# Kernel optimization log

Hardware: AMD Instinct MI355X
Metric: run time of the kernel (lower is better)

The kernel has to match this reference:

```python
import jax, jax.numpy as jnp
import numpy as np

N = 50000   # num nodes
E = 800000  # num edges
D = 128     # embedding dim
EPS = 1e-5


def setup_inputs() -> dict:
    key = jax.random.key(0)
    ks = jax.random.split(key, 16)
    x = jnp.arange(N, dtype=jnp.int32)
    edge_index = jax.random.randint(ks[0], (2, E), 0, N, dtype=jnp.int32)
    weight = jax.random.uniform(ks[1], (E,), dtype=jnp.float32)
    emb = jax.random.normal(ks[2], (N, D), dtype=jnp.float32)
    # layer dims: 128->128, 128->64, 64->32
    dims = [(128, 128), (128, 64), (64, 32)]
    inp = {"x": x, "edge_index": edge_index, "weight": weight, "emb": emb}
    for i, (fi, fo) in enumerate(dims, start=1):
        s = 1.0 / np.sqrt(fi)
        inp[f"W{i}"] = jax.random.uniform(ks[3 * i], (fi, fo), dtype=jnp.float32, minval=-s, maxval=s)
        inp[f"b{i}"] = jnp.zeros((fo,), dtype=jnp.float32)
        inp[f"g{i}"] = jnp.ones((fo,), dtype=jnp.float32)
        inp[f"be{i}"] = jnp.zeros((fo,), dtype=jnp.float32)
    return inp


def _gcn_conv(h, src, dst, w, W, b):
    # PyG GCNConv: linear, add self-loops (weight 1), symmetric normalization, scatter-add
    h = h @ W  # [N, Fout]
    loop = jnp.arange(N, dtype=src.dtype)
    src_l = jnp.concatenate([src, loop])
    dst_l = jnp.concatenate([dst, loop])
    w_l = jnp.concatenate([w, jnp.ones((N,), w.dtype)])
    deg = jax.ops.segment_sum(w_l, dst_l, num_segments=N)
    dinv = jnp.where(deg > 0, jax.lax.rsqrt(jnp.maximum(deg, 1e-30)), 0.0)
    norm = dinv[src_l] * w_l * dinv[dst_l]  # [E+N]
    msg = h[src_l] * norm[:, None]          # gather + scale, [E+N, Fout]
    out = jax.ops.segment_sum(msg, dst_l, num_segments=N)
    return out + b


def _batch_norm(h, g, be):
    mu = h.mean(axis=0)
    var = h.var(axis=0)  # biased, as torch BN uses for normalization
    return (h - mu) * jax.lax.rsqrt(var + EPS) * g + be


def reference(x, edge_index, weight, emb,
              W1, b1, g1, be1,
              W2, b2, g2, be2,
              W3, b3, g3, be3):
    src, dst = edge_index[0], edge_index[1]
    h = emb[x]  # embedding lookup
    h = _batch_norm(_gcn_conv(h, src, dst, weight, W1, b1), g1, be1)
    h = jax.nn.relu(h)
    h = _batch_norm(_gcn_conv(h, src, dst, weight, W2, b2), g2, be2)
    h = jax.nn.relu(h)
    h = _batch_norm(_gcn_conv(h, src, dst, weight, W3, b3), g3, be3)
    return h
```

## Files before the change

### kernel.cpp

```cpp
#include <hip/hip_runtime.h>
#include <hip/hip_bf16.h>

#define BN_EPS 1e-5f
#define FIXSCALE 16777216.0f
#define FIXINV   5.9604644775390625e-08
#define LOWMASK  0xFFFFFFFFFFULL

typedef __attribute__((ext_vector_type(8))) short bf16x8;
typedef __attribute__((ext_vector_type(4))) float f32x4;

__device__ __forceinline__ unsigned short bfu(float v) {
  return __bfloat16_as_ushort(__float2bfloat16(v));
}
__device__ __forceinline__ unsigned int pk_bf2(float a, float b) {
  return (unsigned int)bfu(a) | ((unsigned int)bfu(b) << 16);
}
__device__ __forceinline__ float bf_lo(unsigned int u) { return __uint_as_float(u << 16); }
__device__ __forceinline__ float bf_hi(unsigned int u) { return __uint_as_float(u & 0xFFFF0000u); }

__device__ __forceinline__ void fma8(float* a, uint4 u, float c) {
  a[0] += bf_lo(u.x) * c; a[1] += bf_hi(u.x) * c;
  a[2] += bf_lo(u.y) * c; a[3] += bf_hi(u.y) * c;
  a[4] += bf_lo(u.z) * c; a[5] += bf_hi(u.z) * c;
  a[6] += bf_lo(u.w) * c; a[7] += bf_hi(u.w) * c;
}

__device__ __forceinline__ float4 load4(const float* p) { return *(const float4*)p; }
__device__ __forceinline__ float4 load4(const unsigned short* p) {
  uint2 u = *(const uint2*)p;
  return make_float4(bf_lo(u.x), bf_hi(u.x), bf_lo(u.y), bf_hi(u.y));
}


__global__ void prep_k(const float* __restrict__ W1, const float* __restrict__ W2,
                       const float* __restrict__ W3, unsigned short* __restrict__ wt1,
                       unsigned short* __restrict__ wt2, unsigned short* __restrict__ wt3,
                       unsigned long long* __restrict__ packed, int n) {
  int idx = blockIdx.x * 256 + threadIdx.x;
  if (idx < n) packed[idx] = 0ULL;
  if (idx < 128 * 128) {
    int c = idx >> 7, k = idx & 127;
    wt1[idx] = bfu(W1[k * 128 + c]);
  } else if (idx < 128 * 128 + 128 * 64) {
    int i2 = idx - 128 * 128;
    int c = i2 >> 7, k = i2 & 127;
    wt2[i2] = bfu(W2[k * 64 + c]);
  } else if (idx < 128 * 128 + 128 * 64 + 64 * 32) {
    int i2 = idx - 128 * 128 - 128 * 64;
    int c = i2 >> 6, k = i2 & 63;
    wt3[i2] = bfu(W3[k * 32 + c]);
  }
}


__global__ void hist64_k(const int* __restrict__ dst, const float* __restrict__ w,
                         unsigned long long* __restrict__ packed, int* __restrict__ rank, int e) {
  int i = (blockIdx.x * blockDim.x + threadIdx.x) * 2;
  if (i + 1 < e) {
    int2 d2 = *(const int2*)(dst + i);
    float2 w2 = *(const float2*)(w + i);
    unsigned long long a0 = (1ULL << 40) | (unsigned long long)__float2uint_rn(w2.x * FIXSCALE);
    unsigned long long a1 = (1ULL << 40) | (unsigned long long)__float2uint_rn(w2.y * FIXSCALE);
    unsigned long long o0 = atomicAdd(&packed[d2.x], a0);
    unsigned long long o1 = atomicAdd(&packed[d2.y], a1);
    *(int2*)(rank + i) = make_int2((int)(o0 >> 40), (int)(o1 >> 40));
  } else if (i < e) {
    unsigned long long fw = (unsigned long long)__float2uint_rn(w[i] * FIXSCALE);
    unsigned long long old = atomicAdd(&packed[dst[i]], (1ULL << 40) | fw);
    rank[i] = (int)(old >> 40);
  }
}

__global__ void scan_partial_k(const unsigned long long* __restrict__ packed,
                               int* __restrict__ bsum, float* __restrict__ dinv, int n) {
  __shared__ int s[256];
  int idx = blockIdx.x * 256 + threadIdx.x;
  unsigned long long p = (idx < n) ? packed[idx] : 0ULL;
  if (idx < n)
    dinv[idx] = rsqrtf(1.0f + (float)((double)(p & LOWMASK) * FIXINV));
  s[threadIdx.x] = (int)(p >> 40);
  __syncthreads();
  for (int off = 128; off > 0; off >>= 1) {
    if (threadIdx.x < off) s[threadIdx.x] += s[threadIdx.x + off];
    __syncthreads();
  }
  if (threadIdx.x == 0) bsum[blockIdx.x] = s[0];
}

__global__ void scan_final_k(const unsigned long long* __restrict__ packed,
                             const int* __restrict__ bsum, int* __restrict__ rowptr,
                             int n, int nb) {
  __shared__ int sb[256];
  __shared__ int s[256];
  const int b = blockIdx.x, t = threadIdx.x;

  int bv = (t < nb) ? bsum[t] : 0;
  sb[t] = bv;
  __syncthreads();
  for (int off = 1; off < 256; off <<= 1) {
    int u = (t >= off) ? sb[t - off] : 0;
    __syncthreads();
    sb[t] += u;
    __syncthreads();
  }
  const int blockbase = (b == 0) ? 0 : sb[b - 1];
  if (b == 0 && t == 0) rowptr[n] = sb[nb - 1];

  int idx = b * 256 + t;
  int v = (idx < n) ? (int)(packed[idx] >> 40) : 0;
  s[t] = v;
  __syncthreads();
  for (int off = 1; off < 256; off <<= 1) {
    int u = (t >= off) ? s[t - off] : 0;
    __syncthreads();
    s[t] += u;
    __syncthreads();
  }
  if (idx < n) rowptr[idx] = blockbase + s[t] - v;
}

__global__ void scatter_nb_k(const int* __restrict__ src, const int* __restrict__ dst,
                             const float* __restrict__ w, const int* __restrict__ rank,
                             const float* __restrict__ dinv, const int* __restrict__ rowptr,
                             int2* __restrict__ csr, int e) {
  int i = (blockIdx.x * blockDim.x + threadIdx.x) * 2;
  if (i + 1 < e) {
    int2 s2 = *(const int2*)(src + i);
    int2 d2 = *(const int2*)(dst + i);
    float2 w2 = *(const float2*)(w + i);
    int2 r2 = *(const int2*)(rank + i);
    int p0 = rowptr[d2.x] + r2.x;
    int p1 = rowptr[d2.y] + r2.y;
    csr[p0] = make_int2(s2.x, __float_as_int(dinv[s2.x] * w2.x * dinv[d2.x]));
    csr[p1] = make_int2(s2.y, __float_as_int(dinv[s2.y] * w2.y * dinv[d2.y]));
  } else if (i < e) {
    int d = dst[i], s = src[i];
    int pos = rowptr[d] + rank[i];
    csr[pos] = make_int2(s, __float_as_int(dinv[s] * w[i] * dinv[d]));
  }
}


template <typename TIN, int FIN, int FOUT, bool BNIN, bool GATHER>
__global__ __launch_bounds__(256) void gemm_mfma_k(
    const TIN* __restrict__ H, const int* __restrict__ xidx,
    const float* __restrict__ scale, const float* __restrict__ shift,
    const unsigned short* __restrict__ WtG, unsigned short* __restrict__ out, int n) {
  constexpr int C4 = FIN / 4;
  constexpr int ldH = FIN + 8;
  constexpr int ldW = FIN + 8;
  constexpr int ldC = FOUT + 4;
  constexpr int NCT = FOUT / 16;
  constexpr int NK = FIN / 32;
  constexpr int HT_SH = 64 * ldH;
  constexpr int WT_SH = FOUT * ldW;
  constexpr int STAGE_B = (HT_SH + WT_SH) * 2;
  constexpr int C_B = 64 * ldC * 4;
  constexpr int BYTES = STAGE_B > C_B ? STAGE_B : C_B;

  __shared__ __align__(16) char smem[BYTES];
  unsigned short* Ht = (unsigned short*)smem;
  unsigned short* Wt = (unsigned short*)smem + HT_SH;
  float* Cs = (float*)smem;

  const int t = threadIdx.x;
  const int r0 = blockIdx.x * 64;

  constexpr int NH = 64 * C4 / 256;
#pragma unroll
  for (int i = 0; i < NH; ++i) {
    int idx = t + 256 * i;
    int r = idx / C4, c4 = idx % C4;
    int gr = r0 + r;
    if (gr < n) {
      int srow = GATHER ? xidx[gr] : gr;
      float4 v = load4(H + (size_t)srow * FIN + c4 * 4);
      if (BNIN) {
        float4 sc = *(const float4*)(scale + c4 * 4);
        float4 sh = *(const float4*)(shift + c4 * 4);
        v.x = fmaxf(v.x * sc.x + sh.x, 0.f);
        v.y = fmaxf(v.y * sc.y + sh.y, 0.f);
        v.z = fmaxf(v.z * sc.z + sh.z, 0.f);
        v.w = fmaxf(v.w * sc.w + sh.w, 0.f);
      }
      ushort4 p;
      p.x = bfu(v.x); p.y = bfu(v.y); p.z = bfu(v.z); p.w = bfu(v.w);
      *(ushort4*)&Ht[r * ldH + c4 * 4] = p;
    }
  }
  constexpr int NWU = FOUT * FIN / 8 / 256;
#pragma unroll
  for (int i = 0; i < NWU; ++i) {
    int idx = t + 256 * i;
    int wr = idx / (FIN / 8), w8 = idx % (FIN / 8);
    *(uint4*)&Wt[wr * ldW + w8 * 8] = *(const uint4*)&WtG[wr * FIN + w8 * 8];
  }
  __syncthreads();

  const int w = t >> 6;
  const int l = t & 63;
  const int l15 = l & 15;
  const int kg = l >> 4;
  const int arow = w * 16 + l15;

  f32x4 acc[NCT];
#pragma unroll
  for (int c = 0; c < NCT; ++c) acc[c] = (f32x4){0.f, 0.f, 0.f, 0.f};

#pragma unroll
  for (int kk = 0; kk < NK; ++kk) {
    bf16x8 a = *(const bf16x8*)&Ht[arow * ldH + kk * 32 + kg * 8];
#pragma unroll
    for (int c = 0; c < NCT; ++c) {
      bf16x8 b = *(const bf16x8*)&Wt[(c * 16 + l15) * ldW + kk * 32 + kg * 8];
      acc[c] = __builtin_amdgcn_mfma_f32_16x16x32_bf16(a, b, acc[c], 0, 0, 0);
    }
  }
  __syncthreads();

#pragma unroll
  for (int c = 0; c < NCT; ++c)
#pragma unroll
    for (int m = 0; m < 4; ++m)
      Cs[(w * 16 + kg * 4 + m) * ldC + c * 16 + l15] = acc[c][m];
  __syncthreads();

  constexpr int NU = 64 * FOUT / 8 / 256;
#pragma unroll
  for (int i = 0; i < NU; ++i) {
    int u = t + 256 * i;
    int r = u / (FOUT / 8), c8 = u % (FOUT / 8);
    int gr = r0 + r;
    if (gr < n) {
      const float* p = &Cs[r * ldC + c8 * 8];
      float4 v0 = *(const float4*)p;
      float4 v1 = *(const float4*)(p + 4);
      uint4 o;
      o.x = pk_bf2(v0.x, v0.y); o.y = pk_bf2(v0.z, v0.w);
      o.z = pk_bf2(v1.x, v1.y); o.w = pk_bf2(v1.z, v1.w);
      *(uint4*)&out[(size_t)gr * FOUT + c8 * 8] = o;
    }
  }
}


template <int FOUT>
__global__ void agg_csr_k(const unsigned short* __restrict__ hW, const int* __restrict__ rowptr,
                          const int2* __restrict__ csr, const float* __restrict__ dinv,
                          const float* __restrict__ b, unsigned short* __restrict__ out, int n) {
  constexpr int TPR = FOUT / 8;
  int gid = blockIdx.x * blockDim.x + threadIdx.x;
  int row = gid / TPR, j = gid % TPR;
  if (row >= n) return;

  const float di = dinv[row];
  const float c0 = di * di;
  float a[8];
  {
    uint4 hu = *(const uint4*)(hW + (size_t)row * FOUT + j * 8);
    const float4 bb0 = *(const float4*)(b + j * 8);
    const float4 bb1 = *(const float4*)(b + j * 8 + 4);
    a[0] = bb0.x; a[1] = bb0.y; a[2] = bb0.z; a[3] = bb0.w;
    a[4] = bb1.x; a[5] = bb1.y; a[6] = bb1.z; a[7] = bb1.w;
    fma8(a, hu, c0);
  }

  const int e0 = rowptr[row], e1 = rowptr[row + 1];
  int ee = e0;
  for (; ee + 1 < e1; ee += 2) {
    const int2 d0 = csr[ee];
    const int2 d1 = csr[ee + 1];
    const uint4 u0 = *(const uint4*)(hW + (size_t)d0.x * FOUT + j * 8);
    const uint4 u1 = *(const uint4*)(hW + (size_t)d1.x * FOUT + j * 8);
    fma8(a, u0, __int_as_float(d0.y));
    fma8(a, u1, __int_as_float(d1.y));
  }
  if (ee < e1) {
    const int2 d0 = csr[ee];
    const uint4 u0 = *(const uint4*)(hW + (size_t)d0.x * FOUT + j * 8);
    fma8(a, u0, __int_as_float(d0.y));
  }

  uint4 o;
  o.x = pk_bf2(a[0], a[1]); o.y = pk_bf2(a[2], a[3]);
  o.z = pk_bf2(a[4], a[5]); o.w = pk_bf2(a[6], a[7]);
  *(uint4*)&out[(size_t)row * FOUT + j * 8] = o;
}


template <int FOUT>
__global__ __launch_bounds__(256) void bn_stats_part_k(
    const unsigned short* __restrict__ h, float* __restrict__ psum,
    float* __restrict__ psq, int n) {
  constexpr int TPR = FOUT / 8;
  constexpr int RPB = 256 / TPR;
  const int t = threadIdx.x;
  const int j = t % TPR;
  const int rp = t / TPR;

  float s[8] = {0.f, 0.f, 0.f, 0.f, 0.f, 0.f, 0.f, 0.f};
  float q[8] = {0.f, 0.f, 0.f, 0.f, 0.f, 0.f, 0.f, 0.f};
  for (int r = blockIdx.x * RPB + rp; r < n; r += gridDim.x * RPB) {
    uint4 u = *(const uint4*)(h + (size_t)r * FOUT + j * 8);
    float v[8] = {bf_lo(u.x), bf_hi(u.x), bf_lo(u.y), bf_hi(u.y),
                  bf_lo(u.z), bf_hi(u.z), bf_lo(u.w), bf_hi(u.w)};
#pragma unroll
    for (int k = 0; k < 8; ++k) { s[k] += v[k]; q[k] += v[k] * v[k]; }
  }

  __shared__ float4 ls0[256], ls1[256], lq0[256], lq1[256];
  ls0[t] = make_float4(s[0], s[1], s[2], s[3]);
  ls1[t] = make_float4(s[4], s[5], s[6], s[7]);
  lq0[t] = make_float4(q[0], q[1], q[2], q[3]);
  lq1[t] = make_float4(q[4], q[5], q[6], q[7]);
  __syncthreads();
#pragma unroll
  for (int off = RPB / 2; off > 0; off >>= 1) {
    if (rp < off) {
      int o = off * TPR;
      float4 a, b2;
      a = ls0[t]; b2 = ls0[t + o]; ls0[t] = make_float4(a.x + b2.x, a.y + b2.y, a.z + b2.z, a.w + b2.w);
      a = ls1[t]; b2 = ls1[t + o]; ls1[t] = make_float4(a.x + b2.x, a.y + b2.y, a.z + b2.z, a.w + b2.w);
      a = lq0[t]; b2 = lq0[t + o]; lq0[t] = make_float4(a.x + b2.x, a.y + b2.y, a.z + b2.z, a.w + b2.w);
      a = lq1[t]; b2 = lq1[t + o]; lq1[t] = make_float4(a.x + b2.x, a.y + b2.y, a.z + b2.z, a.w + b2.w);
    }
    __syncthreads();
  }
  if (rp == 0) {
    *(float4*)&psum[(size_t)blockIdx.x * FOUT + j * 8] = ls0[j];
    *(float4*)&psum[(size_t)blockIdx.x * FOUT + j * 8 + 4] = ls1[j];
    *(float4*)&psq[(size_t)blockIdx.x * FOUT + j * 8] = lq0[j];
    *(float4*)&psq[(size_t)blockIdx.x * FOUT + j * 8 + 4] = lq1[j];
  }
}

template <int FOUT>
__global__ __launch_bounds__(256) void bn_finalize2_k(
    const float* __restrict__ psum, const float* __restrict__ psq,
    const float* __restrict__ g, const float* __restrict__ be,
    float* __restrict__ scale, float* __restrict__ shift, int nb, int n) {
  constexpr int TPR = FOUT / 4;
  constexpr int GR = 256 / TPR;
  const int t = threadIdx.x;
  const int j = t % TPR;
  const int gr = t / TPR;

  float4 s = make_float4(0.f, 0.f, 0.f, 0.f);
  float4 q = make_float4(0.f, 0.f, 0.f, 0.f);
  for (int b = gr; b < nb; b += GR) {
    float4 v = *(const float4*)&psum[(size_t)b * FOUT + j * 4];
    float4 u = *(const float4*)&psq[(size_t)b * FOUT + j * 4];
    s.x += v.x; s.y += v.y; s.z += v.z; s.w += v.w;
    q.x += u.x; q.y += u.y; q.z += u.z; q.w += u.w;
  }
  __shared__ float4 ls[256];
  __shared__ float4 lq[256];
  ls[t] = s;
  lq[t] = q;
  __syncthreads();
#pragma unroll
  for (int off = GR / 2; off > 0; off >>= 1) {
    if (gr < off) {
      float4 a = ls[t], b2 = ls[t + off * TPR];
      ls[t] = make_float4(a.x + b2.x, a.y + b2.y, a.z + b2.z, a.w + b2.w);
      float4 c = lq[t], d = lq[t + off * TPR];
      lq[t] = make_float4(c.x + d.x, c.y + d.y, c.z + d.z, c.w + d.w);
    }
    __syncthreads();
  }
  if (gr == 0) {
    float4 s4 = ls[j], q4 = lq[j];
    float inv_n = 1.0f / (float)n;
    float mu[4] = {s4.x * inv_n, s4.y * inv_n, s4.z * inv_n, s4.w * inv_n};
    float qq[4] = {q4.x, q4.y, q4.z, q4.w};
#pragma unroll
    for (int k = 0; k < 4; ++k) {
      int c = j * 4 + k;
      float var = qq[k] * inv_n - mu[k] * mu[k];
      float sc = g[c] * rsqrtf(var + BN_EPS);
      scale[c] = sc;
      shift[c] = be[c] - mu[k] * sc;
    }
  }
}

__global__ void bn_apply32_k(const unsigned short* __restrict__ in,
                             const float* __restrict__ scale, const float* __restrict__ shift,
                             float* __restrict__ out, int n) {
  int gid = blockIdx.x * blockDim.x + threadIdx.x;
  int row = gid >> 2, j = gid & 3;
  if (row >= n) return;
  uint4 u = *(const uint4*)(in + (size_t)row * 32 + j * 8);
  float v[8] = {bf_lo(u.x), bf_hi(u.x), bf_lo(u.y), bf_hi(u.y),
                bf_lo(u.z), bf_hi(u.z), bf_lo(u.w), bf_hi(u.w)};
  const float4 sc0 = *(const float4*)(scale + j * 8);
  const float4 sc1 = *(const float4*)(scale + j * 8 + 4);
  const float4 sh0 = *(const float4*)(shift + j * 8);
  const float4 sh1 = *(const float4*)(shift + j * 8 + 4);
  float4 o0 = make_float4(v[0] * sc0.x + sh0.x, v[1] * sc0.y + sh0.y,
                          v[2] * sc0.z + sh0.z, v[3] * sc0.w + sh0.w);
  float4 o1 = make_float4(v[4] * sc1.x + sh1.x, v[5] * sc1.y + sh1.y,
                          v[6] * sc1.z + sh1.z, v[7] * sc1.w + sh1.w);
  float* p = out + (size_t)row * 32 + j * 8;
  *(float4*)p = o0;
  *(float4*)(p + 4) = o1;
}


static inline size_t pad4(size_t v) { return (v + 3) & ~(size_t)3; }

extern "C" void kernel_launch(void* const* d_in, const int* in_sizes, int n_in,
                              void* d_out, int out_size, void* d_ws, size_t ws_size,
                              hipStream_t stream) {
  const int* x = (const int*)d_in[0];
  const int* ei = (const int*)d_in[1];
  const float* w = (const float*)d_in[2];
  const float* emb = (const float*)d_in[3];
  const float* W1 = (const float*)d_in[4];
  const float* b1 = (const float*)d_in[5];
  const float* g1 = (const float*)d_in[6];
  const float* be1 = (const float*)d_in[7];
  const float* W2 = (const float*)d_in[8];
  const float* b2 = (const float*)d_in[9];
  const float* g2 = (const float*)d_in[10];
  const float* be2 = (const float*)d_in[11];
  const float* W3 = (const float*)d_in[12];
  const float* b3 = (const float*)d_in[13];
  const float* g3 = (const float*)d_in[14];
  const float* be3 = (const float*)d_in[15];

  const int n = in_sizes[0];
  const int e = in_sizes[2];
  const int* src = ei;
  const int* dst = ei + e;

  float* ws = (float*)d_ws;
  size_t off = 0;
  unsigned short* bufA16 = (unsigned short*)(ws + off); off += pad4((size_t)n * 64);
  unsigned short* bufB16 = (unsigned short*)(ws + off); off += pad4((size_t)n * 64);
  unsigned long long* packed = (unsigned long long*)(ws + off); off += pad4((size_t)n * 2);
  float* dinv = ws + off; off += pad4(n);
  int* rowptr = (int*)(ws + off); off += pad4(n + 1);
  int* rank = (int*)(ws + off); off += pad4(e);
  int2* csr = (int2*)(ws + off); off += pad4((size_t)e * 2);
  unsigned short* wt1 = (unsigned short*)(ws + off); off += 128 * 128 / 2;
  unsigned short* wt2 = (unsigned short*)(ws + off); off += 128 * 64 / 2;
  unsigned short* wt3 = (unsigned short*)(ws + off); off += 64 * 32 / 2;
  float* psum = ws + off; off += 256 * 128;
  float* psq = ws + off; off += 256 * 128;
  float* scale = ws + off; off += 128;
  float* shift = ws + off; off += 128;
  int* bsum = (int*)(ws + off); off += 256;

  const int B = 256;
  dim3 blk(B);
  const int nb = (n + 255) / 256;
  const int e2 = (e + 1) / 2;
  const int SB = 256;

  prep_k<<<(n + B - 1) / B, blk, 0, stream>>>(W1, W2, W3, wt1, wt2, wt3, packed, n);
  hist64_k<<<(e2 + B - 1) / B, blk, 0, stream>>>(dst, w, packed, rank, e);
  scan_partial_k<<<nb, blk, 0, stream>>>(packed, bsum, dinv, n);
  scan_final_k<<<nb, blk, 0, stream>>>(packed, bsum, rowptr, n, nb);
  scatter_nb_k<<<(e2 + B - 1) / B, blk, 0, stream>>>(src, dst, w, rank, dinv, rowptr, csr, e);

  const int gx = (n + 63) / 64;

  gemm_mfma_k<float, 128, 128, false, true><<<gx, blk, 0, stream>>>(emb, x, nullptr, nullptr, wt1, bufA16, n);
  agg_csr_k<128><<<((size_t)n * 16 + B - 1) / B, blk, 0, stream>>>(bufA16, rowptr, csr, dinv, b1, bufB16, n);
  bn_stats_part_k<128><<<SB, blk, 0, stream>>>(bufB16, psum, psq, n);
  bn_finalize2_k<128><<<1, blk, 0, stream>>>(psum, psq, g1, be1, scale, shift, SB, n);

  gemm_mfma_k<unsigned short, 128, 64, true, false><<<gx, blk, 0, stream>>>(bufB16, nullptr, scale, shift, wt2, bufA16, n);
  agg_csr_k<64><<<((size_t)n * 8 + B - 1) / B, blk, 0, stream>>>(bufA16, rowptr, csr, dinv, b2, bufB16, n);
  bn_stats_part_k<64><<<SB, blk, 0, stream>>>(bufB16, psum, psq, n);
  bn_finalize2_k<64><<<1, blk, 0, stream>>>(psum, psq, g2, be2, scale, shift, SB, n);

  gemm_mfma_k<unsigned short, 64, 32, true, false><<<gx, blk, 0, stream>>>(bufB16, nullptr, scale, shift, wt3, bufA16, n);
  agg_csr_k<32><<<((size_t)n * 4 + B - 1) / B, blk, 0, stream>>>(bufA16, rowptr, csr, dinv, b3, bufB16, n);
  bn_stats_part_k<32><<<SB, blk, 0, stream>>>(bufB16, psum, psq, n);
  bn_finalize2_k<32><<<1, blk, 0, stream>>>(psum, psq, g3, be3, scale, shift, SB, n);
  bn_apply32_k<<<((size_t)n * 4 + B - 1) / B, blk, 0, stream>>>(bufB16, scale, shift, (float*)d_out, n);
}
```

Measured before the change: 207.4 us.

## Fuse BN stats into aggregation and merge degree histogram with layer-1 GEMM

Each aggregation block now computes per-block partial sums and sums of squares of its fp32 outputs. This removes the separate BN stats pass that re-read the aggregated bf16 tensor. BN finalize becomes one block per column, reducing the now much larger partial buffers. The edge histogram and the layer-1 embedding GEMM are launched as one kernel, split by block index, so they run concurrently and one launch is saved. The trade-offs are many more partial rows written and reduced, and stats now taken from fp32 values rather than the bf16-rounded ones.

```diff
diff --git a/kernel.cpp b/kernel.cpp
--- a/kernel.cpp
+++ b/kernel.cpp
@@ -29,6 +29,13 @@
 __device__ __forceinline__ float4 load4(const unsigned short* p) {
   uint2 u = *(const uint2*)p;
   return make_float4(bf_lo(u.x), bf_hi(u.x), bf_lo(u.y), bf_hi(u.y));
+}
+
+template <int FIN, int FOUT>
+constexpr int gemm_lds_bytes() {
+  int stage = (64 * (FIN + 8) + FOUT * (FIN + 8)) * 2;
+  int cb = 64 * (FOUT + 4) * 4;
+  return stage > cb ? stage : cb;
 }
 
 
@@ -53,9 +60,125 @@
 }
 
 
-__global__ void hist64_k(const int* __restrict__ dst, const float* __restrict__ w,
-                         unsigned long long* __restrict__ packed, int* __restrict__ rank, int e) {
-  int i = (blockIdx.x * blockDim.x + threadIdx.x) * 2;
+template <typename TIN, int FIN, int FOUT, bool BNIN, bool GATHER>
+__device__ __forceinline__ void gemm_body(
+    char* smem, int bid, const TIN* __restrict__ H, const int* __restrict__ xidx,
+    const float* __restrict__ scale, const float* __restrict__ shift,
+    const unsigned short* __restrict__ WtG, unsigned short* __restrict__ out, int n) {
+  constexpr int C4 = FIN / 4;
+  constexpr int ldH = FIN + 8;
+  constexpr int ldW = FIN + 8;
+  constexpr int ldC = FOUT + 4;
+  constexpr int NCT = FOUT / 16;
+  constexpr int NK = FIN / 32;
+  constexpr int HT_SH = 64 * ldH;
+
+  unsigned short* Ht = (unsigned short*)smem;
+  unsigned short* Wt = (unsigned short*)smem + HT_SH;
+  float* Cs = (float*)smem;
+
+  const int t = threadIdx.x;
+  const int r0 = bid * 64;
+
+  constexpr int NH = 64 * C4 / 256;
+#pragma unroll
+  for (int i = 0; i < NH; ++i) {
+    int idx = t + 256 * i;
+    int r = idx / C4, c4 = idx % C4;
+    int gr = r0 + r;
+    if (gr < n) {
+      int srow = GATHER ? xidx[gr] : gr;
+      float4 v = load4(H + (size_t)srow * FIN + c4 * 4);
+      if (BNIN) {
+        float4 sc = *(const float4*)(scale + c4 * 4);
+        float4 sh = *(const float4*)(shift + c4 * 4);
+        v.x = fmaxf(v.x * sc.x + sh.x, 0.f);
+        v.y = fmaxf(v.y * sc.y + sh.y, 0.f);
+        v.z = fmaxf(v.z * sc.z + sh.z, 0.f);
+        v.w = fmaxf(v.w * sc.w + sh.w, 0.f);
+      }
+      ushort4 p;
+      p.x = bfu(v.x); p.y = bfu(v.y); p.z = bfu(v.z); p.w = bfu(v.w);
+      *(ushort4*)&Ht[r * ldH + c4 * 4] = p;
+    }
+  }
+  constexpr int NWU = FOUT * FIN / 8 / 256;
+#pragma unroll
+  for (int i = 0; i < NWU; ++i) {
+    int idx = t + 256 * i;
+    int wr = idx / (FIN / 8), w8 = idx % (FIN / 8);
+    *(uint4*)&Wt[wr * ldW + w8 * 8] = *(const uint4*)&WtG[wr * FIN + w8 * 8];
+  }
+  __syncthreads();
+
+  const int w = t >> 6;
+  const int l = t & 63;
+  const int l15 = l & 15;
+  const int kg = l >> 4;
+  const int arow = w * 16 + l15;
+
+  f32x4 acc[NCT];
+#pragma unroll
+  for (int c = 0; c < NCT; ++c) acc[c] = (f32x4){0.f, 0.f, 0.f, 0.f};
+
+#pragma unroll
+  for (int kk = 0; kk < NK; ++kk) {
+    bf16x8 a = *(const bf16x8*)&Ht[arow * ldH + kk * 32 + kg * 8];
+#pragma unroll
+    for (int c = 0; c < NCT; ++c) {
+      bf16x8 b = *(const bf16x8*)&Wt[(c * 16 + l15) * ldW + kk * 32 + kg * 8];
+      acc[c] = __builtin_amdgcn_mfma_f32_16x16x32_bf16(a, b, acc[c], 0, 0, 0);
+    }
+  }
+  __syncthreads();
+
+#pragma unroll
+  for (int c = 0; c < NCT; ++c)
+#pragma unroll
+    for (int m = 0; m < 4; ++m)
+      Cs[(w * 16 + kg * 4 + m) * ldC + c * 16 + l15] = acc[c][m];
+  __syncthreads();
+
+  constexpr int NU = 64 * FOUT / 8 / 256;
+#pragma unroll
+  for (int i = 0; i < NU; ++i) {
+    int u = t + 256 * i;
+    int r = u / (FOUT / 8), c8 = u % (FOUT / 8);
+    int gr = r0 + r;
+    if (gr < n) {
+      const float* p = &Cs[r * ldC + c8 * 8];
+      float4 v0 = *(const float4*)p;
+      float4 v1 = *(const float4*)(p + 4);
+      uint4 o;
+      o.x = pk_bf2(v0.x, v0.y); o.y = pk_bf2(v0.z, v0.w);
+      o.z = pk_bf2(v1.x, v1.y); o.w = pk_bf2(v1.z, v1.w);
+      *(uint4*)&out[(size_t)gr * FOUT + c8 * 8] = o;
+    }
+  }
+}
+
+template <typename TIN, int FIN, int FOUT, bool BNIN, bool GATHER>
+__global__ __launch_bounds__(256) void gemm_mfma_k(
+    const TIN* __restrict__ H, const int* __restrict__ xidx,
+    const float* __restrict__ scale, const float* __restrict__ shift,
+    const unsigned short* __restrict__ WtG, unsigned short* __restrict__ out, int n) {
+  __shared__ __align__(16) char smem[gemm_lds_bytes<FIN, FOUT>()];
+  gemm_body<TIN, FIN, FOUT, BNIN, GATHER>(smem, blockIdx.x, H, xidx, scale, shift, WtG, out, n);
+}
+
+
+__global__ __launch_bounds__(256) void hist_gemm1_k(
+    const float* __restrict__ emb, const int* __restrict__ x,
+    const unsigned short* __restrict__ wt1, unsigned short* __restrict__ outA,
+    const int* __restrict__ dst, const float* __restrict__ w,
+    unsigned long long* __restrict__ packed, int* __restrict__ rank,
+    int n, int e, int gx) {
+  __shared__ __align__(16) char smem[gemm_lds_bytes<128, 128>()];
+  if ((int)blockIdx.x < gx) {
+    gemm_body<float, 128, 128, false, true>(smem, blockIdx.x, emb, x, nullptr, nullptr, wt1, outA, n);
+    return;
+  }
+  int i = ((blockIdx.x - gx) * 256 + threadIdx.x) * 2;
   if (i + 1 < e) {
     int2 d2 = *(const int2*)(dst + i);
     float2 w2 = *(const float2*)(w + i);
@@ -70,6 +193,7 @@
     rank[i] = (int)(old >> 40);
   }
 }
+
 
 __global__ void scan_partial_k(const unsigned long long* __restrict__ packed,
                                int* __restrict__ bsum, float* __restrict__ dinv, int n) {
@@ -141,188 +265,68 @@
 }
 
 
-template <typename TIN, int FIN, int FOUT, bool BNIN, bool GATHER>
-__global__ __launch_bounds__(256) void gemm_mfma_k(
-    const TIN* __restrict__ H, const int* __restrict__ xidx,
-    const float* __restrict__ scale, const float* __restrict__ shift,
-    const unsigned short* __restrict__ WtG, unsigned short* __restrict__ out, int n) {
-  constexpr int C4 = FIN / 4;
-  constexpr int ldH = FIN + 8;
-  constexpr int ldW = FIN + 8;
-  constexpr int ldC = FOUT + 4;
-  constexpr int NCT = FOUT / 16;
-  constexpr int NK = FIN / 32;
-  constexpr int HT_SH = 64 * ldH;
-  constexpr int WT_SH = FOUT * ldW;
-  constexpr int STAGE_B = (HT_SH + WT_SH) * 2;
-  constexpr int C_B = 64 * ldC * 4;
-  constexpr int BYTES = STAGE_B > C_B ? STAGE_B : C_B;
-
-  __shared__ __align__(16) char smem[BYTES];
-  unsigned short* Ht = (unsigned short*)smem;
-  unsigned short* Wt = (unsigned short*)smem + HT_SH;
-  float* Cs = (float*)smem;
-
-  const int t = threadIdx.x;
-  const int r0 = blockIdx.x * 64;
-
-  constexpr int NH = 64 * C4 / 256;
-#pragma unroll
-  for (int i = 0; i < NH; ++i) {
-    int idx = t + 256 * i;
-    int r = idx / C4, c4 = idx % C4;
-    int gr = r0 + r;
-    if (gr < n) {
-      int srow = GATHER ? xidx[gr] : gr;
-      float4 v = load4(H + (size_t)srow * FIN + c4 * 4);
-      if (BNIN) {
-        float4 sc = *(const float4*)(scale + c4 * 4);
-        float4 sh = *(const float4*)(shift + c4 * 4);
-        v.x = fmaxf(v.x * sc.x + sh.x, 0.f);
-        v.y = fmaxf(v.y * sc.y + sh.y, 0.f);
-        v.z = fmaxf(v.z * sc.z + sh.z, 0.f);
-        v.w = fmaxf(v.w * sc.w + sh.w, 0.f);
-      }
-      ushort4 p;
-      p.x = bfu(v.x); p.y = bfu(v.y); p.z = bfu(v.z); p.w = bfu(v.w);
-      *(ushort4*)&Ht[r * ldH + c4 * 4] = p;
-    }
-  }
-  constexpr int NWU = FOUT * FIN / 8 / 256;
-#pragma unroll
-  for (int i = 0; i < NWU; ++i) {
-    int idx = t + 256 * i;
-    int wr = idx / (FIN / 8), w8 = idx % (FIN / 8);
-    *(uint4*)&Wt[wr * ldW + w8 * 8] = *(const uint4*)&WtG[wr * FIN + w8 * 8];
-  }
-  __syncthreads();
-
-  const int w = t >> 6;
-  const int l = t & 63;
-  const int l15 = l & 15;
-  const int kg = l >> 4;
-  const int arow = w * 16 + l15;
-
-  f32x4 acc[NCT];
-#pragma unroll
-  for (int c = 0; c < NCT; ++c) acc[c] = (f32x4){0.f, 0.f, 0.f, 0.f};
-
-#pragma unroll
-  for (int kk = 0; kk < NK; ++kk) {
-    bf16x8 a = *(const bf16x8*)&Ht[arow * ldH + kk * 32 + kg * 8];
-#pragma unroll
-    for (int c = 0; c < NCT; ++c) {
-      bf16x8 b = *(const bf16x8*)&Wt[(c * 16 + l15) * ldW + kk * 32 + kg * 8];
-      acc[c] = __builtin_amdgcn_mfma_f32_16x16x32_bf16(a, b, acc[c], 0, 0, 0);
-    }
-  }
-  __syncthreads();
-
-#pragma unroll
-  for (int c = 0; c < NCT; ++c)
-#pragma unroll
-    for (int m = 0; m < 4; ++m)
-      Cs[(w * 16 + kg * 4 + m) * ldC + c * 16 + l15] = acc[c][m];
-  __syncthreads();
-
-  constexpr int NU = 64 * FOUT / 8 / 256;
-#pragma unroll
-  for (int i = 0; i < NU; ++i) {
-    int u = t + 256 * i;
-    int r = u / (FOUT / 8), c8 = u % (FOUT / 8);
-    int gr = r0 + r;
-    if (gr < n) {
-      const float* p = &Cs[r * ldC + c8 * 8];
-      float4 v0 = *(const float4*)p;
-      float4 v1 = *(const float4*)(p + 4);
-      uint4 o;
-      o.x = pk_bf2(v0.x, v0.y); o.y = pk_bf2(v0.z, v0.w);
-      o.z = pk_bf2(v1.x, v1.y); o.w = pk_bf2(v1.z, v1.w);
-      *(uint4*)&out[(size_t)gr * FOUT + c8 * 8] = o;
-    }
-  }
-}
-
-
 template <int FOUT>
-__global__ void agg_csr_k(const unsigned short* __restrict__ hW, const int* __restrict__ rowptr,
-                          const int2* __restrict__ csr, const float* __restrict__ dinv,
-                          const float* __restrict__ b, unsigned short* __restrict__ out, int n) {
-  constexpr int TPR = FOUT / 8;
-  int gid = blockIdx.x * blockDim.x + threadIdx.x;
-  int row = gid / TPR, j = gid % TPR;
-  if (row >= n) return;
-
-  const float di = dinv[row];
-  const float c0 = di * di;
-  float a[8];
-  {
-    uint4 hu = *(const uint4*)(hW + (size_t)row * FOUT + j * 8);
-    const float4 bb0 = *(const float4*)(b + j * 8);
-    const float4 bb1 = *(const float4*)(b + j * 8 + 4);
-    a[0] = bb0.x; a[1] = bb0.y; a[2] = bb0.z; a[3] = bb0.w;
-    a[4] = bb1.x; a[5] = bb1.y; a[6] = bb1.z; a[7] = bb1.w;
-    fma8(a, hu, c0);
-  }
-
-  const int e0 = rowptr[row], e1 = rowptr[row + 1];
-  int ee = e0;
-  for (; ee + 1 < e1; ee += 2) {
-    const int2 d0 = csr[ee];
-    const int2 d1 = csr[ee + 1];
-    const uint4 u0 = *(const uint4*)(hW + (size_t)d0.x * FOUT + j * 8);
-    const uint4 u1 = *(const uint4*)(hW + (size_t)d1.x * FOUT + j * 8);
-    fma8(a, u0, __int_as_float(d0.y));
-    fma8(a, u1, __int_as_float(d1.y));
-  }
-  if (ee < e1) {
-    const int2 d0 = csr[ee];
-    const uint4 u0 = *(const uint4*)(hW + (size_t)d0.x * FOUT + j * 8);
-    fma8(a, u0, __int_as_float(d0.y));
-  }
-
-  uint4 o;
-  o.x = pk_bf2(a[0], a[1]); o.y = pk_bf2(a[2], a[3]);
-  o.z = pk_bf2(a[4], a[5]); o.w = pk_bf2(a[6], a[7]);
-  *(uint4*)&out[(size_t)row * FOUT + j * 8] = o;
-}
-
-
-template <int FOUT>
-__global__ __launch_bounds__(256) void bn_stats_part_k(
-    const unsigned short* __restrict__ h, float* __restrict__ psum,
-    float* __restrict__ psq, int n) {
+__global__ __launch_bounds__(256) void agg_csr_k(
+    const unsigned short* __restrict__ hW, const int* __restrict__ rowptr,
+    const int2* __restrict__ csr, const float* __restrict__ dinv,
+    const float* __restrict__ b, unsigned short* __restrict__ out,
+    float* __restrict__ psum, float* __restrict__ psq, int n) {
   constexpr int TPR = FOUT / 8;
   constexpr int RPB = 256 / TPR;
   const int t = threadIdx.x;
   const int j = t % TPR;
   const int rp = t / TPR;
-
-  float s[8] = {0.f, 0.f, 0.f, 0.f, 0.f, 0.f, 0.f, 0.f};
-  float q[8] = {0.f, 0.f, 0.f, 0.f, 0.f, 0.f, 0.f, 0.f};
-  for (int r = blockIdx.x * RPB + rp; r < n; r += gridDim.x * RPB) {
-    uint4 u = *(const uint4*)(h + (size_t)r * FOUT + j * 8);
-    float v[8] = {bf_lo(u.x), bf_hi(u.x), bf_lo(u.y), bf_hi(u.y),
-                  bf_lo(u.z), bf_hi(u.z), bf_lo(u.w), bf_hi(u.w)};
-#pragma unroll
-    for (int k = 0; k < 8; ++k) { s[k] += v[k]; q[k] += v[k] * v[k]; }
+  const int row = blockIdx.x * RPB + rp;
+  const bool valid = row < n;
+
+  float a[8] = {0.f, 0.f, 0.f, 0.f, 0.f, 0.f, 0.f, 0.f};
+  if (valid) {
+    const float di = dinv[row];
+    const float c0 = di * di;
+    {
+      uint4 hu = *(const uint4*)(hW + (size_t)row * FOUT + j * 8);
+      const float4 bb0 = *(const float4*)(b + j * 8);
+      const float4 bb1 = *(const float4*)(b + j * 8 + 4);
+      a[0] = bb0.x; a[1] = bb0.y; a[2] = bb0.z; a[3] = bb0.w;
+      a[4] = bb1.x; a[5] = bb1.y; a[6] = bb1.z; a[7] = bb1.w;
+      fma8(a, hu, c0);
+    }
+    const int e0 = rowptr[row], e1 = rowptr[row + 1];
+    int ee = e0;
+    for (; ee + 1 < e1; ee += 2) {
+      const int2 d0 = csr[ee];
+      const int2 d1 = csr[ee + 1];
+      const uint4 u0 = *(const uint4*)(hW + (size_t)d0.x * FOUT + j * 8);
+      const uint4 u1 = *(const uint4*)(hW + (size_t)d1.x * FOUT + j * 8);
+      fma8(a, u0, __int_as_float(d0.y));
+      fma8(a, u1, __int_as_float(d1.y));
+    }
+    if (ee < e1) {
+      const int2 d0 = csr[ee];
+      const uint4 u0 = *(const uint4*)(hW + (size_t)d0.x * FOUT + j * 8);
+      fma8(a, u0, __int_as_float(d0.y));
+    }
+    uint4 o;
+    o.x = pk_bf2(a[0], a[1]); o.y = pk_bf2(a[2], a[3]);
+    o.z = pk_bf2(a[4], a[5]); o.w = pk_bf2(a[6], a[7]);
+    *(uint4*)&out[(size_t)row * FOUT + j * 8] = o;
   }
 
   __shared__ float4 ls0[256], ls1[256], lq0[256], lq1[256];
-  ls0[t] = make_float4(s[0], s[1], s[2], s[3]);
-  ls1[t] = make_float4(s[4], s[5], s[6], s[7]);
-  lq0[t] = make_float4(q[0], q[1], q[2], q[3]);
-  lq1[t] = make_float4(q[4], q[5], q[6], q[7]);
+  ls0[t] = make_float4(a[0], a[1], a[2], a[3]);
+  ls1[t] = make_float4(a[4], a[5], a[6], a[7]);
+  lq0[t] = make_float4(a[0] * a[0], a[1] * a[1], a[2] * a[2], a[3] * a[3]);
+  lq1[t] = make_float4(a[4] * a[4], a[5] * a[5], a[6] * a[6], a[7] * a[7]);
   __syncthreads();
 #pragma unroll
   for (int off = RPB / 2; off > 0; off >>= 1) {
     if (rp < off) {
       int o = off * TPR;
-      float4 a, b2;
-      a = ls0[t]; b2 = ls0[t + o]; ls0[t] = make_float4(a.x + b2.x, a.y + b2.y, a.z + b2.z, a.w + b2.w);
-      a = ls1[t]; b2 = ls1[t + o]; ls1[t] = make_float4(a.x + b2.x, a.y + b2.y, a.z + b2.z, a.w + b2.w);
-      a = lq0[t]; b2 = lq0[t + o]; lq0[t] = make_float4(a.x + b2.x, a.y + b2.y, a.z + b2.z, a.w + b2.w);
-      a = lq1[t]; b2 = lq1[t + o]; lq1[t] = make_float4(a.x + b2.x, a.y + b2.y, a.z + b2.z, a.w + b2.w);
+      float4 p, q;
+      p = ls0[t]; q = ls0[t + o]; ls0[t] = make_float4(p.x + q.x, p.y + q.y, p.z + q.z, p.w + q.w);
+      p = ls1[t]; q = ls1[t + o]; ls1[t] = make_float4(p.x + q.x, p.y + q.y, p.z + q.z, p.w + q.w);
+      p = lq0[t]; q = lq0[t + o]; lq0[t] = make_float4(p.x + q.x, p.y + q.y, p.z + q.z, p.w + q.w);
+      p = lq1[t]; q = lq1[t + o]; lq1[t] = make_float4(p.x + q.x, p.y + q.y, p.z + q.z, p.w + q.w);
     }
     __syncthreads();
   }
@@ -334,53 +338,34 @@
   }
 }
 
+
 template <int FOUT>
-__global__ __launch_bounds__(256) void bn_finalize2_k(
+__global__ __launch_bounds__(256) void bn_fin_col_k(
     const float* __restrict__ psum, const float* __restrict__ psq,
     const float* __restrict__ g, const float* __restrict__ be,
-    float* __restrict__ scale, float* __restrict__ shift, int nb, int n) {
-  constexpr int TPR = FOUT / 4;
-  constexpr int GR = 256 / TPR;
+    float* __restrict__ scale, float* __restrict__ shift, int nblk, int n) {
+  const int col = blockIdx.x;
   const int t = threadIdx.x;
-  const int j = t % TPR;
-  const int gr = t / TPR;
-
-  float4 s = make_float4(0.f, 0.f, 0.f, 0.f);
-  float4 q = make_float4(0.f, 0.f, 0.f, 0.f);
-  for (int b = gr; b < nb; b += GR) {
-    float4 v = *(const float4*)&psum[(size_t)b * FOUT + j * 4];
-    float4 u = *(const float4*)&psq[(size_t)b * FOUT + j * 4];
-    s.x += v.x; s.y += v.y; s.z += v.z; s.w += v.w;
-    q.x += u.x; q.y += u.y; q.z += u.z; q.w += u.w;
-  }
-  __shared__ float4 ls[256];
-  __shared__ float4 lq[256];
-  ls[t] = s;
-  lq[t] = q;
-  __syncthreads();
-#pragma unroll
-  for (int off = GR / 2; off > 0; off >>= 1) {
-    if (gr < off) {
-      float4 a = ls[t], b2 = ls[t + off * TPR];
-      ls[t] = make_float4(a.x + b2.x, a.y + b2.y, a.z + b2.z, a.w + b2.w);
-      float4 c = lq[t], d = lq[t + off * TPR];
-      lq[t] = make_float4(c.x + d.x, c.y + d.y, c.z + d.z, c.w + d.w);
-    }
-    __syncthreads();
-  }
-  if (gr == 0) {
-    float4 s4 = ls[j], q4 = lq[j];
+  float s = 0.f, q = 0.f;
+  for (int i = t; i < nblk; i += 256) {
+    s += psum[(size_t)i * FOUT + col];
+    q += psq[(size_t)i * FOUT + col];
+  }
+  __shared__ float ss[256], qq[256];
+  ss[t] = s;
+  qq[t] = q;
+  __syncthreads();
+  for (int off = 128; off > 0; off >>= 1) {
+    if (t < off) { ss[t] += ss[t + off]; qq[t] += qq[t + off]; }
+    __syncthreads();
+  }
+  if (t == 0) {
     float inv_n = 1.0f / (float)n;
-    float mu[4] = {s4.x * inv_n, s4.y * inv_n, s4.z * inv_n, s4.w * inv_n};
-    float qq[4] = {q4.x, q4.y, q4.z, q4.w};
-#pragma unroll
-    for (int k = 0; k < 4; ++k) {
-      int c = j * 4 + k;
-      float var = qq[k] * inv_n - mu[k] * mu[k];
-      float sc = g[c] * rsqrtf(var + BN_EPS);
-      scale[c] = sc;
-      shift[c] = be[c] - mu[k] * sc;
-    }
+    float mu = ss[0] * inv_n;
+    float var = qq[0] * inv_n - mu * mu;
+    float sc = g[col] * rsqrtf(var + BN_EPS);
+    scale[col] = sc;
+    shift[col] = be[col] - mu * sc;
   }
 }
 
@@ -446,8 +431,8 @@
   unsigned short* wt1 = (unsigned short*)(ws + off); off += 128 * 128 / 2;
   unsigned short* wt2 = (unsigned short*)(ws + off); off += 128 * 64 / 2;
   unsigned short* wt3 = (unsigned short*)(ws + off); off += 64 * 32 / 2;
-  float* psum = ws + off; off += 256 * 128;
-  float* psq = ws + off; off += 256 * 128;
+  float* psum = ws + off; off += 400384;
+  float* psq = ws + off; off += 400384;
   float* scale = ws + off; off += 128;
   float* shift = ws + off; off += 128;
   int* bsum = (int*)(ws + off); off += 256;
@@ -456,29 +441,26 @@
   dim3 blk(B);
   const int nb = (n + 255) / 256;
   const int e2 = (e + 1) / 2;
-  const int SB = 256;
+  const int gx = (n + 63) / 64;
+  const int nblk1 = (n + 15) / 16;
+  const int nblk2 = (n + 31) / 32;
+  const int nblk3 = (n + 63) / 64;
 
   prep_k<<<(n + B - 1) / B, blk, 0, stream>>>(W1, W2, W3, wt1, wt2, wt3, packed, n);
-  hist64_k<<<(e2 + B - 1) / B, blk, 0, stream>>>(dst, w, packed, rank, e);
+  hist_gemm1_k<<<gx + (e2 + B - 1) / B, blk, 0, stream>>>(emb, x, wt1, bufA16, dst, w, packed, rank, n, e, gx);
   scan_partial_k<<<nb, blk, 0, stream>>>(packed, bsum, dinv, n);
   scan_final_k<<<nb, blk, 0, stream>>>(packed, bsum, rowptr, n, nb);
   scatter_nb_k<<<(e2 + B - 1) / B, blk, 0, stream>>>(src, dst, w, rank, dinv, rowptr, csr, e);
 
-  const int gx = (n + 63) / 64;
-
-  gemm_mfma_k<float, 128, 128, false, true><<<gx, blk, 0, stream>>>(emb, x, nullptr, nullptr, wt1, bufA16, n);
-  agg_csr_k<128><<<((size_t)n * 16 + B - 1) / B, blk, 0, stream>>>(bufA16, rowptr, csr, dinv, b1, bufB16, n);
-  bn_stats_part_k<128><<<SB, blk, 0, stream>>>(bufB16, psum, psq, n);
-  bn_finalize2_k<128><<<1, blk, 0, stream>>>(psum, psq, g1, be1, scale, shift, SB, n);
+  agg_csr_k<128><<<nblk1, blk, 0, stream>>>(bufA16, rowptr, csr, dinv, b1, bufB16, psum, psq, n);
+  bn_fin_col_k<128><<<128, blk, 0, stream>>>(psum, psq, g1, be1, scale, shift, nblk1, n);
 
   gemm_mfma_k<unsigned short, 128, 64, true, false><<<gx, blk, 0, stream>>>(bufB16, nullptr, scale, shift, wt2, bufA16, n);
-  agg_csr_k<64><<<((size_t)n * 8 + B - 1) / B, blk, 0, stream>>>(bufA16, rowptr, csr, dinv, b2, bufB16, n);
-  bn_stats_part_k<64><<<SB, blk, 0, stream>>>(bufB16, psum, psq, n);
-  bn_finalize2_k<64><<<1, blk, 0, stream>>>(psum, psq, g2, be2, scale, shift, SB, n);
+  agg_csr_k<64><<<nblk2, blk, 0, stream>>>(bufA16, rowptr, csr, dinv, b2, bufB16, psum, psq, n);
+  bn_fin_col_k<64><<<64, blk, 0, stream>>>(psum, psq, g2, be2, scale, shift, nblk2, n);
 
   gemm_mfma_k<unsigned short, 64, 32, true, false><<<gx, blk, 0, stream>>>(bufB16, nullptr, scale, shift, wt3, bufA16, n);
-  agg_csr_k<32><<<((size_t)n * 4 + B - 1) / B, blk, 0, stream>>>(bufA16, rowptr, csr, dinv, b3, bufB16, n);
-  bn_stats_part_k<32><<<SB, blk, 0, stream>>>(bufB16, psum, psq, n);
-  bn_finalize2_k<32><<<1, blk, 0, stream>>>(psum, psq, g3, be3, scale, shift, SB, n);
+  agg_csr_k<32><<<nblk3, blk, 0, stream>>>(bufA16, rowptr, csr, dinv, b3, bufB16, psum, psq, n);
+  bn_fin_col_k<32><<<32, blk, 0, stream>>>(psum, psq, g3, be3, scale, shift, nblk3, n);
   bn_apply32_k<<<((size_t)n * 4 + B - 1) / B, blk, 0, stream>>>(bufB16, scale, shift, (float*)d_out, n);
 }
```

New measurement: 188.0 us. 9.3% less time.
